# Performance work log

Hardware: AMD Instinct MI355X
Metric: run time of the kernel (lower is better)

Reference implementation:

```python
import jax, jax.numpy as jnp
import numpy as np

EMBED_DIM = 12  # hardcoded in the original module


def setup_inputs() -> dict:
    key = jax.random.key(0)
    k_x, k_w, k_b, k_v = jax.random.split(key, 4)
    feature_dim = 768
    hidden_dim = 4
    feature_num = feature_dim // EMBED_DIM  # 64 fields
    batch = 32768
    x = jax.random.normal(k_x, (batch, feature_dim), dtype=jnp.float32)
    # nn.Linear(feature_dim, 1): weight [1, feature_dim], bias [1]
    W = jax.random.normal(k_w, (1, feature_dim), dtype=jnp.float32) / np.sqrt(feature_dim)
    b = jax.random.normal(k_b, (1,), dtype=jnp.float32) * 0.01
    # V: [feature_num, field_num, hidden_dim]
    V = jax.random.normal(k_v, (feature_num, feature_num, hidden_dim), dtype=jnp.float32)
    return {"x": x, "W": W, "b": b, "V": V}


def reference(x, W, b, V):
    B, D = x.shape
    F = V.shape[0]               # feature_num == field_num
    E = D // F                   # embedding_dim (12)
    # linear part: [B, 1]
    linear_part = x @ W.T + b
    # Pairwise interaction coefficients: C[i, j] = <V[i, j], V[j, i]>
    C = jnp.sum(V * jnp.swapaxes(V, 0, 1), axis=-1)          # [F, F]
    M = C * jnp.triu(jnp.ones((F, F), dtype=x.dtype), k=1)   # keep i < j only
    # sum_{i<j} (x_i . x_j) * C[i,j]  ==  sum_{j,e} Xr[b,j,e] * (sum_i Xr[b,i,e] * M[i,j])
    Xr = x.reshape(B, F, E)                                    # [B, F, E]
    T = jnp.einsum('bie,ij->bje', Xr, M)                       # [B, F, E]
    interaction = jnp.sum(Xr * T, axis=(1, 2))[:, None]        # [B, 1]
    return jax.nn.sigmoid(linear_part + interaction)
```

## Files before the change

kernel.cpp:

```cpp
#include <hip/hip_runtime.h>
#include <hip/hip_bf16.h>

#define BATCH 32768
#define NF    64
#define NE    12
#define MB    16
#define MROWS (MB*NE)
#define LSTR  68
#define NTILE (BATCH/MB)
#define GRID  512
#define TPB   (NTILE/GRID)

typedef __attribute__((ext_vector_type(8))) short short8;
typedef __attribute__((ext_vector_type(4))) float float4v;

#define WS_SHT 0
#define WS_SLT 8192

__device__ __forceinline__ short bfb(float v) {
    union { __hip_bfloat16 h; short s; } u;
    u.h = __float2bfloat16(v);
    return u.s;
}

__global__ void prep_kernel(const float* __restrict__ V,
                            unsigned short* __restrict__ ShT,
                            unsigned short* __restrict__ SlT) {
    const int idx = blockIdx.x * 256 + threadIdx.x;
    if (idx < NF * NF) {
        const int i = idx >> 6, j = idx & 63;
        const float4v a = *(const float4v*)(V + (size_t)((i << 6) | j) * 4);
        const float4v b = *(const float4v*)(V + (size_t)((j << 6) | i) * 4);
        const float s = (i == j) ? 0.0f
                      : 0.5f * (a.x * b.x + a.y * b.y + a.z * b.z + a.w * b.w);
        const __hip_bfloat16 sh = __float2bfloat16(s);
        union { __hip_bfloat16 h; unsigned short u; } uh, ul;
        uh.h = sh; ul.h = __float2bfloat16(s - __bfloat162float(sh));
        ShT[(j << 6) | i] = uh.u;
        SlT[(j << 6) | i] = ul.u;
    }
}

__global__ __launch_bounds__(256, 2) void ffm_mfma(
    const float* __restrict__ x,
    const float* __restrict__ W,
    const float* __restrict__ bvec,
    const unsigned short* __restrict__ ShT,
    const unsigned short* __restrict__ SlT,
    float* __restrict__ out)
{
    __shared__ float Xs[MROWS * LSTR];
    __shared__ float red[MROWS];
    __shared__ float Wl[NF * NE];

    const int tid  = threadIdx.x;
    const int w    = tid >> 6;
    const int lane = tid & 63;
    const int l15  = lane & 15;
    const int q    = lane >> 4;

    #pragma unroll
    for (int k = 0; k < 3; ++k) Wl[k * 256 + tid] = W[k * 256 + tid];

    const float bias = bvec[0];

    short8 shf[4][2], slf[4][2];
    #pragma unroll
    for (int ns = 0; ns < 4; ++ns)
        #pragma unroll
        for (int kb = 0; kb < 2; ++kb) {
            const int off = ((ns << 4) + l15) * 64 + kb * 32 + q * 8;
            shf[ns][kb] = *(const short8*)(ShT + off);
            slf[ns][kb] = *(const short8*)(SlT + off);
        }

    int lofs[12];
    #pragma unroll
    for (int p = 0; p < 12; ++p) {
        const int fid = p * 256 + tid;
        const int b   = fid / 192;
        const int c4  = fid - b * 192;
        const int d0  = c4 * 4;
        const int i0  = d0 / 12;
        const int e0  = d0 - i0 * 12;
        lofs[p] = (b * NE + e0) * LSTR + i0;
    }

    float4v v[12];
    {
        const float4v* xg = (const float4v*)(x + (size_t)blockIdx.x * MB * (NF * NE));
        #pragma unroll
        for (int p = 0; p < 12; ++p) v[p] = xg[p * 256 + tid];
    }

    for (int tt = 0; tt < TPB; ++tt) {
        const int tile = tt * GRID + blockIdx.x;

        #pragma unroll
        for (int p = 0; p < 12; ++p) {
            float* dst = Xs + lofs[p];
            dst[0 * LSTR] = v[p].x; dst[1 * LSTR] = v[p].y;
            dst[2 * LSTR] = v[p].z; dst[3 * LSTR] = v[p].w;
        }
        __syncthreads();

        if (tt + 1 < TPB) {
            const int ntile = (tt + 1) * GRID + blockIdx.x;
            const float4v* xg = (const float4v*)(x + (size_t)ntile * MB * (NF * NE));
            #pragma unroll
            for (int p = 0; p < 12; ++p) v[p] = xg[p * 256 + tid];
        }

        #pragma unroll
        for (int ms = 0; ms < 3; ++ms) {
            const int msg  = w * 3 + ms;
            const int mrow = (msg << 4) + l15;

            short8 ah[2], al[2];
            #pragma unroll
            for (int kb = 0; kb < 2; ++kb) {
                const float4v t0 = *(const float4v*)(Xs + mrow * LSTR + kb * 32 + q * 8);
                const float4v t1 = *(const float4v*)(Xs + mrow * LSTR + kb * 32 + q * 8 + 4);
                const float a8[8] = {t0.x, t0.y, t0.z, t0.w, t1.x, t1.y, t1.z, t1.w};
                #pragma unroll
                for (int j = 0; j < 8; ++j) {
                    const float vv = a8[j];
                    const __hip_bfloat16 h = __float2bfloat16(vv);
                    ah[kb][j] = bfb(vv);
                    al[kb][j] = bfb(vv - __bfloat162float(h));
                }
            }

            const int c0 = ((ms + q) % 3) * 4;
            float4v acc[4];
            #pragma unroll
            for (int ns = 0; ns < 4; ++ns)
                acc[ns] = *(const float4v*)(Wl + ((ns << 4) + l15) * 12 + c0);

            #pragma unroll
            for (int ns = 0; ns < 4; ++ns) {
                float4v c = acc[ns];
                c = __builtin_amdgcn_mfma_f32_16x16x32_bf16(ah[0], shf[ns][0], c, 0, 0, 0);
                c = __builtin_amdgcn_mfma_f32_16x16x32_bf16(ah[1], shf[ns][1], c, 0, 0, 0);
                c = __builtin_amdgcn_mfma_f32_16x16x32_bf16(al[0], shf[ns][0], c, 0, 0, 0);
                c = __builtin_amdgcn_mfma_f32_16x16x32_bf16(al[1], shf[ns][1], c, 0, 0, 0);
                c = __builtin_amdgcn_mfma_f32_16x16x32_bf16(ah[0], slf[ns][0], c, 0, 0, 0);
                c = __builtin_amdgcn_mfma_f32_16x16x32_bf16(ah[1], slf[ns][1], c, 0, 0, 0);
                acc[ns] = c;
            }

            #pragma unroll
            for (int rg = 0; rg < 4; ++rg) {
                const int m = (msg << 4) + (q << 2) + rg;
                float p = 0.0f;
                #pragma unroll
                for (int ns = 0; ns < 4; ++ns) {
                    const int n = (ns << 4) + l15;
                    p = fmaf(Xs[m * LSTR + n], acc[ns][rg], p);
                }
                p += __shfl_xor(p, 1);
                p += __shfl_xor(p, 2);
                p += __shfl_xor(p, 4);
                p += __shfl_xor(p, 8);
                if (l15 == 0) red[m] = p;
            }
        }
        __syncthreads();

        if (tid < MB) {
            float s = 0.0f;
            #pragma unroll
            for (int e = 0; e < NE; ++e) s += red[tid * NE + e];
            const float z = s + bias;
            out[tile * MB + tid] = 1.0f / (1.0f + __expf(-z));
        }
    }
}

extern "C" void kernel_launch(void* const* d_in, const int* in_sizes, int n_in,
                              void* d_out, int out_size, void* d_ws, size_t ws_size,
                              hipStream_t stream) {
    const float* x  = (const float*)d_in[0];
    const float* W  = (const float*)d_in[1];
    const float* bb = (const float*)d_in[2];
    const float* V  = (const float*)d_in[3];
    unsigned short* ShT = (unsigned short*)((char*)d_ws + WS_SHT);
    unsigned short* SlT = (unsigned short*)((char*)d_ws + WS_SLT);
    float* out = (float*)d_out;

    prep_kernel<<<dim3(16), dim3(256), 0, stream>>>(V, ShT, SlT);
    ffm_mfma<<<dim3(GRID), dim3(256), 0, stream>>>(x, W, bb, ShT, SlT, out);
}
```

Measured before the change: 155.1 us.

## Fuse pairwise-coefficient prep into main kernel, building bf16 split matrices in LDS

Drops the separate prep kernel. Each block now computes the symmetric interaction coefficients from V and stores their hi/lo bf16 split into shared memory, reusing the X tile buffer before the main loop, then loads its MFMA operand fragments from there. This removes one kernel launch and the round trip through the workspace. In exchange, every block redundantly reads V, about 64KB per block served mostly from L2, and runs extra setup compute and barriers. The LDS store of each X tile also moves to the end of the previous iteration.

```diff
diff --git a/kernel.cpp b/kernel.cpp
--- a/kernel.cpp
+++ b/kernel.cpp
@@ -7,15 +7,13 @@
 #define MB    16
 #define MROWS (MB*NE)
 #define LSTR  68
+#define SSTR  72
 #define NTILE (BATCH/MB)
 #define GRID  512
 #define TPB   (NTILE/GRID)
 
 typedef __attribute__((ext_vector_type(8))) short short8;
 typedef __attribute__((ext_vector_type(4))) float float4v;
-
-#define WS_SHT 0
-#define WS_SLT 8192
 
 __device__ __forceinline__ short bfb(float v) {
     union { __hip_bfloat16 h; short s; } u;
@@ -23,35 +21,19 @@
     return u.s;
 }
 
-__global__ void prep_kernel(const float* __restrict__ V,
-                            unsigned short* __restrict__ ShT,
-                            unsigned short* __restrict__ SlT) {
-    const int idx = blockIdx.x * 256 + threadIdx.x;
-    if (idx < NF * NF) {
-        const int i = idx >> 6, j = idx & 63;
-        const float4v a = *(const float4v*)(V + (size_t)((i << 6) | j) * 4);
-        const float4v b = *(const float4v*)(V + (size_t)((j << 6) | i) * 4);
-        const float s = (i == j) ? 0.0f
-                      : 0.5f * (a.x * b.x + a.y * b.y + a.z * b.z + a.w * b.w);
-        const __hip_bfloat16 sh = __float2bfloat16(s);
-        union { __hip_bfloat16 h; unsigned short u; } uh, ul;
-        uh.h = sh; ul.h = __float2bfloat16(s - __bfloat162float(sh));
-        ShT[(j << 6) | i] = uh.u;
-        SlT[(j << 6) | i] = ul.u;
-    }
-}
-
-__global__ __launch_bounds__(256, 2) void ffm_mfma(
+__global__ __launch_bounds__(256, 2) void ffm_fused(
     const float* __restrict__ x,
     const float* __restrict__ W,
     const float* __restrict__ bvec,
-    const unsigned short* __restrict__ ShT,
-    const unsigned short* __restrict__ SlT,
+    const float* __restrict__ V,
     float* __restrict__ out)
 {
-    __shared__ float Xs[MROWS * LSTR];
+    __shared__ __align__(16) float Xs[MROWS * LSTR];
     __shared__ float red[MROWS];
     __shared__ float Wl[NF * NE];
+
+    unsigned short* Sh = (unsigned short*)Xs;
+    unsigned short* Sl = Sh + NF * SSTR;
 
     const int tid  = threadIdx.x;
     const int w    = tid >> 6;
@@ -59,20 +41,57 @@
     const int l15  = lane & 15;
     const int q    = lane >> 4;
 
+    float4v v[12];
+    {
+        const float4v* xg = (const float4v*)(x + (size_t)blockIdx.x * MB * (NF * NE));
+        #pragma unroll
+        for (int p = 0; p < 12; ++p) v[p] = xg[p * 256 + tid];
+    }
+
+    const float bias = bvec[0];
+
     #pragma unroll
     for (int k = 0; k < 3; ++k) Wl[k * 256 + tid] = W[k * 256 + tid];
 
-    const float bias = bvec[0];
+    {
+        const int n  = tid >> 2;
+        const int kq = tid & 3;
+        float sv[16];
+        #pragma unroll
+        for (int c = 0; c < 16; ++c) {
+            const int k = kq * 16 + c;
+            const float4v a = *(const float4v*)(V + (size_t)((k << 6) | n) * 4);
+            const float4v b = *(const float4v*)(V + (size_t)((n << 6) | k) * 4);
+            sv[c] = (n == k) ? 0.0f
+                  : 0.5f * (a.x * b.x + a.y * b.y + a.z * b.z + a.w * b.w);
+        }
+        short8 ph0, ph1, pl0, pl1;
+        #pragma unroll
+        for (int j = 0; j < 8; ++j) {
+            const float s0 = sv[j], s1 = sv[8 + j];
+            const __hip_bfloat16 h0 = __float2bfloat16(s0);
+            const __hip_bfloat16 h1 = __float2bfloat16(s1);
+            ph0[j] = bfb(s0); pl0[j] = bfb(s0 - __bfloat162float(h0));
+            ph1[j] = bfb(s1); pl1[j] = bfb(s1 - __bfloat162float(h1));
+        }
+        const int so = n * SSTR + kq * 16;
+        *(short8*)(Sh + so)     = ph0;
+        *(short8*)(Sh + so + 8) = ph1;
+        *(short8*)(Sl + so)     = pl0;
+        *(short8*)(Sl + so + 8) = pl1;
+    }
+    __syncthreads();
 
     short8 shf[4][2], slf[4][2];
     #pragma unroll
     for (int ns = 0; ns < 4; ++ns)
         #pragma unroll
         for (int kb = 0; kb < 2; ++kb) {
-            const int off = ((ns << 4) + l15) * 64 + kb * 32 + q * 8;
-            shf[ns][kb] = *(const short8*)(ShT + off);
-            slf[ns][kb] = *(const short8*)(SlT + off);
-        }
+            const int ro = ((ns << 4) + l15) * SSTR + kb * 32 + q * 8;
+            shf[ns][kb] = *(const short8*)(Sh + ro);
+            slf[ns][kb] = *(const short8*)(Sl + ro);
+        }
+    __syncthreads();
 
     int lofs[12];
     #pragma unroll
@@ -86,23 +105,16 @@
         lofs[p] = (b * NE + e0) * LSTR + i0;
     }
 
-    float4v v[12];
-    {
-        const float4v* xg = (const float4v*)(x + (size_t)blockIdx.x * MB * (NF * NE));
-        #pragma unroll
-        for (int p = 0; p < 12; ++p) v[p] = xg[p * 256 + tid];
-    }
+    #pragma unroll
+    for (int p = 0; p < 12; ++p) {
+        float* dst = Xs + lofs[p];
+        dst[0 * LSTR] = v[p].x; dst[1 * LSTR] = v[p].y;
+        dst[2 * LSTR] = v[p].z; dst[3 * LSTR] = v[p].w;
+    }
+    __syncthreads();
 
     for (int tt = 0; tt < TPB; ++tt) {
         const int tile = tt * GRID + blockIdx.x;
-
-        #pragma unroll
-        for (int p = 0; p < 12; ++p) {
-            float* dst = Xs + lofs[p];
-            dst[0 * LSTR] = v[p].x; dst[1 * LSTR] = v[p].y;
-            dst[2 * LSTR] = v[p].z; dst[3 * LSTR] = v[p].w;
-        }
-        __syncthreads();
 
         if (tt + 1 < TPB) {
             const int ntile = (tt + 1) * GRID + blockIdx.x;
@@ -174,6 +186,16 @@
             const float z = s + bias;
             out[tile * MB + tid] = 1.0f / (1.0f + __expf(-z));
         }
+
+        if (tt + 1 < TPB) {
+            #pragma unroll
+            for (int p = 0; p < 12; ++p) {
+                float* dst = Xs + lofs[p];
+                dst[0 * LSTR] = v[p].x; dst[1 * LSTR] = v[p].y;
+                dst[2 * LSTR] = v[p].z; dst[3 * LSTR] = v[p].w;
+            }
+            __syncthreads();
+        }
     }
 }
 
@@ -184,10 +206,7 @@
     const float* W  = (const float*)d_in[1];
     const float* bb = (const float*)d_in[2];
     const float* V  = (const float*)d_in[3];
-    unsigned short* ShT = (unsigned short*)((char*)d_ws + WS_SHT);
-    unsigned short* SlT = (unsigned short*)((char*)d_ws + WS_SLT);
     float* out = (float*)d_out;
 
-    prep_kernel<<<dim3(16), dim3(256), 0, stream>>>(V, ShT, SlT);
-    ffm_mfma<<<dim3(GRID), dim3(256), 0, stream>>>(x, W, bb, ShT, SlT, out);
+    ffm_fused<<<dim3(GRID), dim3(256), 0, stream>>>(x, W, bb, V, out);
 }
```

Result: slower. 161.5 us (+4.2%).

## Make each wavefront own its batch rows and drop block-wide barriers

Applied to the files above, without the earlier changes.

Remaps the global load and LDS scatter so each wavefront writes exactly the 4 batch rows (48 M-rows) that it later consumes in its MFMA tiles. This lets the main loop drop both __syncthreads per tile and rely on wavefront-local ordering. The final reduction is also reworked: a shorter shuffle chain, a per-wave reduction through red4/redP in LDS, and per-wave output writes. The gain depends on the LDS writes and reads within a wavefront being ordered without an explicit barrier or waitcnt. If that ordering does not hold, the results could race.

```diff
diff --git a/kernel.cpp b/kernel.cpp
--- a/kernel.cpp
+++ b/kernel.cpp
@@ -49,8 +49,9 @@
     const unsigned short* __restrict__ SlT,
     float* __restrict__ out)
 {
-    __shared__ float Xs[MROWS * LSTR];
-    __shared__ float red[MROWS];
+    __shared__ __align__(16) float Xs[MROWS * LSTR];
+    __shared__ __align__(16) float red4[MROWS * 4];
+    __shared__ __align__(16) float redP[MROWS];
     __shared__ float Wl[NF * NE];
 
     const int tid  = threadIdx.x;
@@ -59,8 +60,13 @@
     const int l15  = lane & 15;
     const int q    = lane >> 4;
 
-    #pragma unroll
-    for (int k = 0; k < 3; ++k) Wl[k * 256 + tid] = W[k * 256 + tid];
+    float4v v[12];
+    {
+        const float4v* xg = (const float4v*)x;
+        const size_t base = (size_t)blockIdx.x * 3072 + w * 768 + lane;
+        #pragma unroll
+        for (int p = 0; p < 12; ++p) v[p] = xg[base + p * 64];
+    }
 
     const float bias = bvec[0];
 
@@ -74,23 +80,20 @@
             slf[ns][kb] = *(const short8*)(SlT + off);
         }
 
+    #pragma unroll
+    for (int k = 0; k < 3; ++k) Wl[k * 256 + tid] = W[k * 256 + tid];
+    __syncthreads();
+
     int lofs[12];
     #pragma unroll
     for (int p = 0; p < 12; ++p) {
-        const int fid = p * 256 + tid;
-        const int b   = fid / 192;
-        const int c4  = fid - b * 192;
-        const int d0  = c4 * 4;
-        const int i0  = d0 / 12;
-        const int e0  = d0 - i0 * 12;
-        lofs[p] = (b * NE + e0) * LSTR + i0;
-    }
-
-    float4v v[12];
-    {
-        const float4v* xg = (const float4v*)(x + (size_t)blockIdx.x * MB * (NF * NE));
-        #pragma unroll
-        for (int p = 0; p < 12; ++p) v[p] = xg[p * 256 + tid];
+        const int f0   = p * 256 + lane * 4;
+        const int brow = f0 / 768;
+        const int r    = f0 - brow * 768;
+        const int i0   = r / 12;
+        const int e0   = r - i0 * 12;
+        const int m    = (4 * w + brow) * NE + e0;
+        lofs[p] = m * LSTR + i0;
     }
 
     for (int tt = 0; tt < TPB; ++tt) {
@@ -102,13 +105,13 @@
             dst[0 * LSTR] = v[p].x; dst[1 * LSTR] = v[p].y;
             dst[2 * LSTR] = v[p].z; dst[3 * LSTR] = v[p].w;
         }
-        __syncthreads();
 
         if (tt + 1 < TPB) {
             const int ntile = (tt + 1) * GRID + blockIdx.x;
-            const float4v* xg = (const float4v*)(x + (size_t)ntile * MB * (NF * NE));
-            #pragma unroll
-            for (int p = 0; p < 12; ++p) v[p] = xg[p * 256 + tid];
+            const float4v* xg = (const float4v*)x;
+            const size_t base = (size_t)ntile * 3072 + w * 768 + lane;
+            #pragma unroll
+            for (int p = 0; p < 12; ++p) v[p] = xg[base + p * 64];
         }
 
         #pragma unroll
@@ -160,19 +163,27 @@
                 }
                 p += __shfl_xor(p, 1);
                 p += __shfl_xor(p, 2);
-                p += __shfl_xor(p, 4);
-                p += __shfl_xor(p, 8);
-                if (l15 == 0) red[m] = p;
-            }
-        }
-        __syncthreads();
-
-        if (tid < MB) {
-            float s = 0.0f;
-            #pragma unroll
-            for (int e = 0; e < NE; ++e) s += red[tid * NE + e];
-            const float z = s + bias;
-            out[tile * MB + tid] = 1.0f / (1.0f + __expf(-z));
+                if ((l15 & 3) == 0) red4[m * 4 + (l15 >> 2)] = p;
+            }
+        }
+
+        {
+            float pm = 0.0f;
+            if (lane < 48) {
+                const float4v r4 = *(const float4v*)(red4 + (48 * w + lane) * 4);
+                pm = r4.x + r4.y + r4.z + r4.w;
+                redP[48 * w + lane] = pm;
+            }
+            if (lane < 4) {
+                const float* rp = redP + 48 * w + lane * 12;
+                const float4v a = *(const float4v*)(rp);
+                const float4v b = *(const float4v*)(rp + 4);
+                const float4v c = *(const float4v*)(rp + 8);
+                const float s = (a.x + a.y + a.z + a.w)
+                              + (b.x + b.y + b.z + b.w)
+                              + (c.x + c.y + c.z + c.w) + bias;
+                out[tile * MB + w * 4 + lane] = 1.0f / (1.0f + __expf(-s));
+            }
         }
     }
 }
```

New measurement: 154.7 us, median of 2. Within noise of the previous version (-0.2%).
